# Kernel tuning notes

Measured on AMD Instinct MI355X. Metric: run time of the kernel, lower is better.

The kernel has to match this reference:

```python
import jax, jax.numpy as jnp
import numpy as np

EPS = 1e-5
GROUPS = 4


def gconv1x1(x, w, b, groups):
    # x: [B,C,H,W]; w: [Cout, Cin//groups]; grouped 1x1 conv
    B, C, H, W = x.shape
    Co = w.shape[0]
    xg = x.reshape(B, groups, C // groups, H, W)
    wg = w.reshape(groups, Co // groups, C // groups)
    y = jnp.einsum('bgchw,goc->bgohw', xg, wg).reshape(B, Co, H, W)
    if b is not None:
        y = y + b[None, :, None, None]
    return y


def setup_inputs() -> dict:
    key = jax.random.key(0)
    ks = jax.random.split(key, 9)
    B, C, H, W = 8, 64, 160, 160
    Cq = C // 8
    s = 0.1
    return {
        'x': jax.random.normal(ks[0], (B, C, H, W), jnp.float32),
        'wq': jax.random.normal(ks[1], (Cq, C // GROUPS), jnp.float32) * s,
        'bq': jax.random.normal(ks[2], (Cq,), jnp.float32) * s,
        'wk': jax.random.normal(ks[3], (Cq, C // GROUPS), jnp.float32) * s,
        'bk': jax.random.normal(ks[4], (Cq,), jnp.float32) * s,
        'wv': jax.random.normal(ks[5], (C, C // GROUPS), jnp.float32) * s,
        'bv': jax.random.normal(ks[6], (C,), jnp.float32) * s,
        'gamma': jax.random.normal(ks[7], (1,), jnp.float32) * s,
        'w1d': jax.random.normal(ks[8], (C, C // GROUPS), jnp.float32) * s,
        'bn_w': jnp.ones((C,), jnp.float32),
        'bn_b': jnp.zeros((C,), jnp.float32),
    }


def reference(x, wq, bq, wk, bk, wv, bv, gamma, w1d, bn_w, bn_b):
    B, C, H, W = x.shape
    q = gconv1x1(x, wq, bq, GROUPS)   # [B,Cq,H,W]
    k = gconv1x1(x, wk, bk, GROUPS)   # [B,Cq,H,W]
    v = gconv1x1(x, wv, bv, GROUPS)   # [B,C,H,W]

    # column (H) attention energies with -inf diagonal (self excluded on H path)
    energy_H = jnp.einsum('bchw,bcjw->bhwj', q, k)  # [B,H,W,H]
    diag = jnp.where(jnp.eye(H, dtype=bool), -jnp.inf, 0.0).astype(x.dtype)
    energy_H = energy_H + diag[:, None, :]
    # row (W) attention energies
    energy_W = jnp.einsum('bchw,bchj->bhwj', q, k)  # [B,H,W,W]

    att = jax.nn.softmax(jnp.concatenate([energy_H, energy_W], axis=3), axis=3)
    att_H = att[..., :H]           # [B,H,W,H]
    att_W = att[..., H:]           # [B,H,W,W]

    out_H = jnp.einsum('bcjw,bhwj->bchw', v, att_H)
    out_W = jnp.einsum('bchj,bhwj->bchw', v, att_W)
    out = gamma[0] * (out_H + out_W)               # [B,C,H,W]

    # kernel-size-1 grouped conv1d (dilation irrelevant for k=1), no bias
    L = H * W
    o = out.reshape(B, GROUPS, C // GROUPS, L)
    w1g = w1d.reshape(GROUPS, C // GROUPS, C // GROUPS)
    o = jnp.einsum('bgcl,goc->bgol', o, w1g).reshape(B, C, L)

    # BatchNorm1d (training mode: batch stats over (B, L), biased variance)
    mean = jnp.mean(o, axis=(0, 2), keepdims=True)
    var = jnp.mean((o - mean) ** 2, axis=(0, 2), keepdims=True)
    o = (o - mean) / jnp.sqrt(var + EPS) * bn_w[None, :, None] + bn_b[None, :, None]

    o = o.reshape(B, C, H, W)
    return jax.nn.relu(o + x)
```

## Files before the change

### kernel.cpp

```cpp
#include <hip/hip_runtime.h>
#include <math.h>

#define B_ 8
#define C_ 64
#define H_ 160
#define W_ 160
#define HW_ (H_*W_)

typedef _Float16 h2 __attribute__((ext_vector_type(2)));
typedef _Float16 h8 __attribute__((ext_vector_type(8)));
typedef float f4v __attribute__((ext_vector_type(4)));
union H8u { h8 v; h2 h[4]; };

__device__ inline float fdot2(h2 a, h2 b, float c) {
    return __builtin_amdgcn_fdot2(a, b, c, false);
}
__device__ inline float dot16(const float4* xr, const float* wr, float acc) {
    float4 a = xr[0], b = xr[1], c = xr[2], d = xr[3];
    acc += a.x*wr[0]  + a.y*wr[1]  + a.z*wr[2]  + a.w*wr[3];
    acc += b.x*wr[4]  + b.y*wr[5]  + b.z*wr[6]  + b.w*wr[7];
    acc += c.x*wr[8]  + c.y*wr[9]  + c.z*wr[10] + c.w*wr[11];
    acc += d.x*wr[12] + d.y*wr[13] + d.z*wr[14] + d.w*wr[15];
    return acc;
}

static constexpr size_t N_PIX  = (size_t)B_*H_*W_;
static constexpr size_t N_FULL = (size_t)B_*H_*W_*C_;
static constexpr size_t OFF_OUTH  = 0;
static constexpr size_t OFF_VROW  = N_FULL/2;
static constexpr size_t OFF_QROW  = OFF_VROW + N_FULL/2;
static constexpr size_t OFF_KROW  = OFF_QROW + N_PIX*4;
static constexpr size_t OFF_MH    = OFF_KROW + N_PIX*4;
static constexpr size_t OFF_SH    = OFF_MH + N_PIX;
static constexpr size_t OFF_BNSUM = OFF_SH + N_PIX;
static constexpr size_t OFF_BNSQ  = OFF_BNSUM + 64;
static constexpr size_t OFF_SCALE = OFF_BNSQ + 64;
static constexpr size_t OFF_SHIFT = OFF_SCALE + 64;

__global__ __launch_bounds__(256,4) void qkv_kernel(
    const float* __restrict__ x,
    const float* __restrict__ wq, const float* __restrict__ bq,
    const float* __restrict__ wk, const float* __restrict__ bk,
    const float* __restrict__ wv, const float* __restrict__ bv,
    _Float16* __restrict__ qrow, _Float16* __restrict__ krow,
    _Float16* __restrict__ vrow)
{
    __shared__ __align__(16) float xs[128][68];
    const int tid = threadIdx.x;
    const int w0 = blockIdx.x * 32;
    const int h0 = blockIdx.y * 4;
    const int b  = blockIdx.z;

    const float* xb = x + (size_t)b*C_*HW_;
    for (int i = tid; i < 2048; i += 256) {
        int c = i >> 5, hh = (i >> 3) & 3, w4 = i & 7;
        float4 v = *(const float4*)(xb + (size_t)c*HW_ + (size_t)(h0+hh)*W_ + w0 + w4*4);
        int pix = hh*32 + w4*4;
        xs[pix+0][c] = v.x; xs[pix+1][c] = v.y; xs[pix+2][c] = v.z; xs[pix+3][c] = v.w;
    }
    __syncthreads();

    float resv[32];
    {
        const int cp = tid & 31, pg = tid >> 5;
        const int c0 = 2*cp, g = c0 >> 4;
        float w0r[16], w1r[16];
        #pragma unroll
        for (int p = 0; p < 4; p++) {
            *(float4*)&w0r[4*p] = ((const float4*)(wv + c0*16))[p];
            *(float4*)&w1r[4*p] = ((const float4*)(wv + (c0+1)*16))[p];
        }
        const float b0 = bv[c0], b1 = bv[c0+1];
        #pragma unroll 4
        for (int i = 0; i < 16; i++) {
            int pix = pg*16 + i;
            const float4* xr = (const float4*)&xs[pix][g*16];
            resv[2*i]   = dot16(xr, w0r, b0);
            resv[2*i+1] = dot16(xr, w1r, b1);
        }
    }
    float resqk[8];
    {
        const int out = tid & 15, pg = tid >> 4;
        const int cq = out & 7, g = cq >> 1;
        const float* wp = ((out < 8) ? wq : wk) + cq*16;
        const float bb = (out < 8) ? bq[cq] : bk[cq];
        float wr[16];
        #pragma unroll
        for (int p = 0; p < 4; p++) *(float4*)&wr[4*p] = ((const float4*)wp)[p];
        #pragma unroll
        for (int i = 0; i < 8; i++) {
            int pix = pg*8 + i;
            resqk[i] = dot16((const float4*)&xs[pix][g*16], wr, bb);
        }
    }
    __syncthreads();

    unsigned* vs32 = (unsigned*)&xs[0][0];
    unsigned* qk32 = vs32 + 4096;
    {
        const int cp = tid & 31, pg = tid >> 5;
        #pragma unroll
        for (int i = 0; i < 16; i++) {
            int pix = pg*16 + i;
            h2 p; p.x = (_Float16)resv[2*i]; p.y = (_Float16)resv[2*i+1];
            vs32[pix*32 + cp] = *(unsigned*)&p;
        }
    }
    {
        const int out = tid & 15, pg = tid >> 4;
        _Float16* qks = (_Float16*)qk32;
        #pragma unroll
        for (int i = 0; i < 8; i++) qks[(pg*8+i)*16 + out] = (_Float16)resqk[i];
    }
    __syncthreads();

    unsigned* vrow32 = (unsigned*)vrow;
    for (int i = tid; i < 4096; i += 256) {
        int pix = i >> 5, cp = i & 31;
        size_t bp = ((size_t)b*H_ + h0 + (pix>>5))*W_ + w0 + (pix & 31);
        vrow32[bp*32 + cp] = vs32[i];
    }
    unsigned* qrow32 = (unsigned*)qrow;
    unsigned* krow32 = (unsigned*)krow;
    for (int i = tid; i < 1024; i += 256) {
        int pix = i >> 3, part = i & 7;
        size_t bp = ((size_t)b*H_ + h0 + (pix>>5))*W_ + w0 + (pix & 31);
        unsigned val = qk32[pix*8 + part];
        if (part < 4) qrow32[bp*4 + part]     = val;
        else          krow32[bp*4 + part - 4] = val;
    }
}

__global__ __launch_bounds__(256,4) void passA_kernel(
    const _Float16* __restrict__ qrow, const _Float16* __restrict__ krow,
    const _Float16* __restrict__ vrow,
    _Float16* __restrict__ outH, float* __restrict__ mH, float* __restrict__ sH)
{
    __shared__ __align__(16) h2 v2[64][84];
    __shared__ __align__(16) _Float16 q2h[160][8];
    __shared__ __align__(16) _Float16 k2h[160][8];
    __shared__ __align__(16) h2 Pt[32][84];

    const int tid = threadIdx.x;
    const int b = blockIdx.x / W_;
    const int w = blockIdx.x % W_;

    if (tid < 160) {
        size_t bp = ((size_t)b*H_ + tid)*W_ + w;
        *(int4*)&q2h[tid][0] = *(const int4*)(qrow + bp*8);
        *(int4*)&k2h[tid][0] = *(const int4*)(krow + bp*8);
    }
    {
        const unsigned* vr32 = (const unsigned*)vrow;
        const int cp = tid & 31, hp0 = tid >> 5;
        #pragma unroll 2
        for (int it = 0; it < 10; it++) {
            int hp = hp0 + 8*it;
            size_t bp0 = (size_t)b*HW_ + (size_t)(2*hp)*W_ + w;
            unsigned u0 = vr32[bp0*32 + cp];
            unsigned u1 = vr32[(bp0 + W_)*32 + cp];
            unsigned e  = __builtin_amdgcn_perm(u1, u0, 0x05040100);
            unsigned o  = __builtin_amdgcn_perm(u1, u0, 0x07060302);
            *(unsigned*)&v2[2*cp][hp]   = e;
            *(unsigned*)&v2[2*cp+1][hp] = o;
        }
    }
    __syncthreads();

    const int u    = tid & 7;
    const int wl   = tid >> 3;
    const int lane = tid & 63;
    const int wid  = tid >> 6;
    const int cM   = wid*16 + (lane & 15);
    const int m_   = lane & 15;
    const int dq   = lane >> 4;

    for (int t = 0; t < 5; t++) {
        const int qh = t*32 + wl;
        H8u qr; qr.v = *(const h8*)&q2h[qh][0];
        float ev[20];
        float mloc = -1e30f;
        #pragma unroll 2
        for (int p = 0; p < 10; p++) {
            int j0 = 2*(u + 8*p);
            H8u ka; ka.v = *(const h8*)&k2h[j0][0];
            H8u kb; kb.v = *(const h8*)&k2h[j0+1][0];
            float e0 = 0.f, e1 = 0.f;
            #pragma unroll
            for (int i = 0; i < 4; i++) {
                e0 = fdot2(qr.h[i], ka.h[i], e0);
                e1 = fdot2(qr.h[i], kb.h[i], e1);
            }
            ev[2*p] = e0; ev[2*p+1] = e1;
            if (j0   != qh) mloc = fmaxf(mloc, e0);
            if (j0+1 != qh) mloc = fmaxf(mloc, e1);
        }
        mloc = fmaxf(mloc, __shfl_xor(mloc, 1));
        mloc = fmaxf(mloc, __shfl_xor(mloc, 2));
        mloc = fmaxf(mloc, __shfl_xor(mloc, 4));
        float sloc = 0.f;
        #pragma unroll
        for (int p = 0; p < 10; p++) {
            int j0 = 2*(u + 8*p);
            float p0 = (j0   == qh) ? 0.f : __expf(ev[2*p]   - mloc);
            float p1 = (j0+1 == qh) ? 0.f : __expf(ev[2*p+1] - mloc);
            sloc += p0 + p1;
            h2 pp; pp.x = (_Float16)p0; pp.y = (_Float16)p1;
            Pt[wl][u + 8*p] = pp;
        }
        sloc += __shfl_xor(sloc, 1);
        sloc += __shfl_xor(sloc, 2);
        sloc += __shfl_xor(sloc, 4);
        if (u == 0) {
            mH[((size_t)b*W_ + w)*H_ + qh] = mloc;
            sH[((size_t)b*W_ + w)*H_ + qh] = sloc;
        }
        __syncthreads();

        f4v acc0 = {0.f,0.f,0.f,0.f}, acc1 = {0.f,0.f,0.f,0.f};
        #pragma unroll
        for (int kt = 0; kt < 5; kt++) {
            const int off = 64*kt + 16*dq;
            h8 bfr = *(const h8*)((const char*)&v2[cM][0] + off);
            h8 a0  = *(const h8*)((const char*)&Pt[m_][0] + off);
            h8 a1  = *(const h8*)((const char*)&Pt[16 + m_][0] + off);
            acc0 = __builtin_amdgcn_mfma_f32_16x16x32_f16(a0, bfr, acc0, 0, 0, 0);
            acc1 = __builtin_amdgcn_mfma_f32_16x16x32_f16(a1, bfr, acc1, 0, 0, 0);
        }
        #pragma unroll
        for (int r = 0; r < 4; r++) {
            int r0 = t*32 + dq*4 + r;
            outH[(((size_t)b*H_ + r0     )*W_ + w)*64 + cM] = (_Float16)acc0[r];
            outH[(((size_t)b*H_ + r0 + 16)*W_ + w)*64 + cM] = (_Float16)acc1[r];
        }
        __syncthreads();
    }
}

__global__ __launch_bounds__(256,4) void passB_kernel(
    const _Float16* __restrict__ qrow, const _Float16* __restrict__ krow,
    const _Float16* vrow,
    const float* __restrict__ gamma, const float* __restrict__ w1d,
    const _Float16* __restrict__ outH, const float* __restrict__ mH, const float* __restrict__ sH,
    _Float16* o16, float* __restrict__ bnsum, float* __restrict__ bnsq)
{
    __shared__ __align__(16) h2 v2[64][84];
    __shared__ __align__(16) _Float16 q2h[160][8];
    __shared__ __align__(16) _Float16 k2h[160][8];
    __shared__ __align__(16) h2 Pt[32][84];
    __shared__ float fHs[32], fWs[32];

    const int tid = threadIdx.x;
    const int b = blockIdx.x / H_;
    const int h = blockIdx.x % H_;
    const float gam = gamma[0];

    const int lane = tid & 63;
    const int wid  = tid >> 6;
    const int cM   = wid*16 + (lane & 15);
    const int m_   = lane & 15;
    const int dq   = lane >> 4;

    float w1dr[16];
    #pragma unroll
    for (int p = 0; p < 4; p++) *(float4*)&w1dr[4*p] = ((const float4*)(w1d + cM*16))[p];

    const size_t rowbase = ((size_t)b*H_ + h)*W_;
    if (tid < 160) {
        size_t bp = rowbase + tid;
        *(int4*)&q2h[tid][0] = *(const int4*)(qrow + bp*8);
        *(int4*)&k2h[tid][0] = *(const int4*)(krow + bp*8);
    }
    {
        const unsigned* vr32 = (const unsigned*)vrow;
        const int cp = tid & 31, wp0 = tid >> 5;
        #pragma unroll 2
        for (int it = 0; it < 10; it++) {
            int wp = wp0 + 8*it;
            size_t bp0 = rowbase + 2*wp;
            unsigned u0 = vr32[bp0*32 + cp];
            unsigned u1 = vr32[(bp0 + 1)*32 + cp];
            unsigned e  = __builtin_amdgcn_perm(u1, u0, 0x05040100);
            unsigned o  = __builtin_amdgcn_perm(u1, u0, 0x07060302);
            *(unsigned*)&v2[2*cp][wp]   = e;
            *(unsigned*)&v2[2*cp+1][wp] = o;
        }
    }
    __syncthreads();

    const int u  = tid & 7;
    const int wl = tid >> 3;
    float bnS = 0.f, bnS2 = 0.f;

    for (int t = 0; t < 5; t++) {
        float oh0[4], oh1[4];
        #pragma unroll
        for (int r = 0; r < 4; r++) {
            int rw0 = t*32 + dq*4 + r;
            oh0[r] = (float)outH[(rowbase + rw0     )*64 + cM];
            oh1[r] = (float)outH[(rowbase + rw0 + 16)*64 + cM];
        }

        const int qw = t*32 + wl;
        H8u qr; qr.v = *(const h8*)&q2h[qw][0];
        float ev[20];
        float mloc = -1e30f;
        #pragma unroll 2
        for (int p = 0; p < 10; p++) {
            int j0 = 2*(u + 8*p);
            H8u ka; ka.v = *(const h8*)&k2h[j0][0];
            H8u kb; kb.v = *(const h8*)&k2h[j0+1][0];
            float e0 = 0.f, e1 = 0.f;
            #pragma unroll
            for (int i = 0; i < 4; i++) {
                e0 = fdot2(qr.h[i], ka.h[i], e0);
                e1 = fdot2(qr.h[i], kb.h[i], e1);
            }
            ev[2*p] = e0; ev[2*p+1] = e1;
            mloc = fmaxf(mloc, e0);
            mloc = fmaxf(mloc, e1);
        }
        mloc = fmaxf(mloc, __shfl_xor(mloc, 1));
        mloc = fmaxf(mloc, __shfl_xor(mloc, 2));
        mloc = fmaxf(mloc, __shfl_xor(mloc, 4));
        float sloc = 0.f;
        #pragma unroll
        for (int p = 0; p < 10; p++) {
            float p0 = __expf(ev[2*p]   - mloc);
            float p1 = __expf(ev[2*p+1] - mloc);
            sloc += p0 + p1;
            h2 pp; pp.x = (_Float16)p0; pp.y = (_Float16)p1;
            Pt[wl][u + 8*p] = pp;
        }
        sloc += __shfl_xor(sloc, 1);
        sloc += __shfl_xor(sloc, 2);
        sloc += __shfl_xor(sloc, 4);
        if (u == 0) {
            float mHv = mH[((size_t)b*W_ + qw)*H_ + h];
            float sHv = sH[((size_t)b*W_ + qw)*H_ + h];
            float M   = fmaxf(mHv, mloc);
            float eH  = __expf(mHv - M), eW = __expf(mloc - M);
            float inv = gam / (sHv*eH + sloc*eW);
            fHs[wl] = eH * inv;
            fWs[wl] = eW * inv;
        }
        __syncthreads();

        f4v acc0 = {0.f,0.f,0.f,0.f}, acc1 = {0.f,0.f,0.f,0.f};
        #pragma unroll
        for (int kt = 0; kt < 5; kt++) {
            const int off = 64*kt + 16*dq;
            h8 bfr = *(const h8*)((const char*)&v2[cM][0] + off);
            h8 a0  = *(const h8*)((const char*)&Pt[m_][0] + off);
            h8 a1  = *(const h8*)((const char*)&Pt[16 + m_][0] + off);
            acc0 = __builtin_amdgcn_mfma_f32_16x16x32_f16(a0, bfr, acc0, 0, 0, 0);
            acc1 = __builtin_amdgcn_mfma_f32_16x16x32_f16(a1, bfr, acc1, 0, 0, 0);
        }
        __syncthreads();

        float* stage = (float*)&Pt[0][0];
        #pragma unroll
        for (int r = 0; r < 4; r++) {
            int rl0 = dq*4 + r, rl1 = rl0 + 16;
            stage[rl0*68 + cM] = oh0[r]*fHs[rl0] + acc0[r]*fWs[rl0];
            stage[rl1*68 + cM] = oh1[r]*fHs[rl1] + acc1[r]*fWs[rl1];
        }
        #pragma unroll
        for (int r = 0; r < 4; r++) {
            #pragma unroll
            for (int mt = 0; mt < 2; mt++) {
                int rl = dq*4 + r + 16*mt;
                int rw = t*32 + rl;
                const float4* sp = (const float4*)&stage[rl*68 + 16*wid];
                float o = 0.f;
                #pragma unroll
                for (int p = 0; p < 4; p++) {
                    float4 sv = sp[p];
                    o += sv.x*w1dr[4*p] + sv.y*w1dr[4*p+1] + sv.z*w1dr[4*p+2] + sv.w*w1dr[4*p+3];
                }
                o16[(rowbase + rw)*64 + cM] = (_Float16)o;
                bnS  += o;
                bnS2 += o*o;
            }
        }
        __syncthreads();
    }
    bnS  += __shfl_xor(bnS, 16);  bnS  += __shfl_xor(bnS, 32);
    bnS2 += __shfl_xor(bnS2, 16); bnS2 += __shfl_xor(bnS2, 32);
    if (dq == 0) {
        atomicAdd(&bnsum[cM], bnS);
        atomicAdd(&bnsq[cM],  bnS2);
    }
}

__global__ void bnfin_kernel(const float* __restrict__ sum, const float* __restrict__ sq,
                             const float* __restrict__ bn_w, const float* __restrict__ bn_b,
                             float* __restrict__ scale, float* __restrict__ shift)
{
    int c = threadIdx.x;
    if (c < C_) {
        const float cnt = (float)(B_*H_*W_);
        float mean = sum[c] / cnt;
        float var  = sq[c] / cnt - mean*mean;
        float istd = rsqrtf(var + 1e-5f);
        float scl  = bn_w[c] * istd;
        scale[c] = scl;
        shift[c] = bn_b[c] - mean*scl;
    }
}

__global__ __launch_bounds__(256) void final_kernel(
    const float* __restrict__ x, const _Float16* __restrict__ o16,
    const float* __restrict__ scale, const float* __restrict__ shift,
    float* __restrict__ out)
{
    __shared__ _Float16 olds[160*66];
    __shared__ float sc[64], sh[64];
    const int tid = threadIdx.x;
    const int b = blockIdx.x / H_, h = blockIdx.x % H_;
    if (tid < 64) { sc[tid] = scale[tid]; sh[tid] = shift[tid]; }
    const unsigned* op = (const unsigned*)(o16 + ((size_t)b*H_ + h)*W_*64);
    unsigned* ol32 = (unsigned*)olds;
    for (int i = tid; i < 5120; i += 256) {
        int w = i >> 5, c2 = i & 31;
        ol32[w*33 + c2] = op[i];
    }
    __syncthreads();
    const float* xr = x   + (size_t)b*C_*HW_ + (size_t)h*W_;
    float*       ob = out + (size_t)b*C_*HW_ + (size_t)h*W_;
    for (int i = tid; i < 64*160; i += 256) {
        int c = i / 160, w = i - c*160;
        float v = (float)olds[w*66 + c] * sc[c] + sh[c] + xr[(size_t)c*HW_ + w];
        ob[(size_t)c*HW_ + w] = fmaxf(v, 0.f);
    }
}

extern "C" void kernel_launch(void* const* d_in, const int* in_sizes, int n_in,
                              void* d_out, int out_size, void* d_ws, size_t ws_size,
                              hipStream_t stream)
{
    (void)in_sizes; (void)n_in; (void)out_size; (void)ws_size;
    const float* x     = (const float*)d_in[0];
    const float* wq    = (const float*)d_in[1];
    const float* bq    = (const float*)d_in[2];
    const float* wk    = (const float*)d_in[3];
    const float* bk    = (const float*)d_in[4];
    const float* wv    = (const float*)d_in[5];
    const float* bv    = (const float*)d_in[6];
    const float* gamma = (const float*)d_in[7];
    const float* w1d   = (const float*)d_in[8];
    const float* bn_w  = (const float*)d_in[9];
    const float* bn_b  = (const float*)d_in[10];

    float* ws = (float*)d_ws;
    _Float16* outH16 = (_Float16*)(ws + OFF_OUTH);
    _Float16* vrow   = (_Float16*)(ws + OFF_VROW);
    _Float16* qrow   = (_Float16*)(ws + OFF_QROW);
    _Float16* krow   = (_Float16*)(ws + OFF_KROW);
    float* mH    = ws + OFF_MH;
    float* sH    = ws + OFF_SH;
    float* bnsum = ws + OFF_BNSUM;
    float* bnsq  = ws + OFF_BNSQ;
    float* scale = ws + OFF_SCALE;
    float* shift = ws + OFF_SHIFT;
    _Float16* o16 = vrow;

    hipMemsetAsync(bnsum, 0, 128*sizeof(float), stream);

    dim3 qgrid(W_/32, H_/4, B_);
    qkv_kernel<<<qgrid, 256, 0, stream>>>(x, wq, bq, wk, bk, wv, bv, qrow, krow, vrow);
    passA_kernel<<<B_*W_, 256, 0, stream>>>(qrow, krow, vrow, outH16, mH, sH);
    passB_kernel<<<B_*H_, 256, 0, stream>>>(qrow, krow, vrow, gamma, w1d,
                                            outH16, mH, sH, o16, bnsum, bnsq);
    bnfin_kernel<<<1, 64, 0, stream>>>(bnsum, bnsq, bn_w, bn_b, scale, shift);
    final_kernel<<<B_*H_, 256, 0, stream>>>(x, o16, scale, shift, (float*)d_out);
}
```

Baseline: 252.5 us.

## Retile LDS fragments for MFMA, stage conv in fp16 per wave, fold BN finalize

After: 244.0 us. 3.4% less time.

```diff
diff --git a/kernel.cpp b/kernel.cpp
--- a/kernel.cpp
+++ b/kernel.cpp
@@ -34,8 +34,6 @@
 static constexpr size_t OFF_SH    = OFF_MH + N_PIX;
 static constexpr size_t OFF_BNSUM = OFF_SH + N_PIX;
 static constexpr size_t OFF_BNSQ  = OFF_BNSUM + 64;
-static constexpr size_t OFF_SCALE = OFF_BNSQ + 64;
-static constexpr size_t OFF_SHIFT = OFF_SCALE + 64;
 
 __global__ __launch_bounds__(256,4) void qkv_kernel(
     const float* __restrict__ x,
@@ -53,7 +51,9 @@
 
     const float* xb = x + (size_t)b*C_*HW_;
     for (int i = tid; i < 2048; i += 256) {
-        int c = i >> 5, hh = (i >> 3) & 3, w4 = i & 7;
+        int w4 = i & 7;
+        int c  = ((i >> 3) & 7) | (((i >> 6) & 7) << 3);
+        int hh = i >> 9;
         float4 v = *(const float4*)(xb + (size_t)c*HW_ + (size_t)(h0+hh)*W_ + w0 + w4*4);
         int pix = hh*32 + w4*4;
         xs[pix+0][c] = v.x; xs[pix+1][c] = v.y; xs[pix+2][c] = v.z; xs[pix+3][c] = v.w;
@@ -137,10 +137,10 @@
     const _Float16* __restrict__ vrow,
     _Float16* __restrict__ outH, float* __restrict__ mH, float* __restrict__ sH)
 {
-    __shared__ __align__(16) h2 v2[64][84];
+    __shared__ __align__(16) _Float16 v2s[5*4*64*8];
+    __shared__ __align__(16) _Float16 Pts[5*4*32*8];
     __shared__ __align__(16) _Float16 q2h[160][8];
     __shared__ __align__(16) _Float16 k2h[160][8];
-    __shared__ __align__(16) h2 Pt[32][84];
 
     const int tid = threadIdx.x;
     const int b = blockIdx.x / W_;
@@ -157,13 +157,15 @@
         #pragma unroll 2
         for (int it = 0; it < 10; it++) {
             int hp = hp0 + 8*it;
-            size_t bp0 = (size_t)b*HW_ + (size_t)(2*hp)*W_ + w;
+            int kt = hp >> 4, dqv = (hp >> 2) & 3, jj = 2*(hp & 3);
+            size_t bp0 = ((size_t)b*H_ + 2*hp)*W_ + w;
             unsigned u0 = vr32[bp0*32 + cp];
             unsigned u1 = vr32[(bp0 + W_)*32 + cp];
             unsigned e  = __builtin_amdgcn_perm(u1, u0, 0x05040100);
             unsigned o  = __builtin_amdgcn_perm(u1, u0, 0x07060302);
-            *(unsigned*)&v2[2*cp][hp]   = e;
-            *(unsigned*)&v2[2*cp+1][hp] = o;
+            int base = ((kt*4 + dqv)*64 + 2*cp)*8 + jj;
+            *(unsigned*)&v2s[base]     = e;
+            *(unsigned*)&v2s[base + 8] = o;
         }
     }
     __syncthreads();
@@ -183,7 +185,7 @@
         float mloc = -1e30f;
         #pragma unroll 2
         for (int p = 0; p < 10; p++) {
-            int j0 = 2*(u + 8*p);
+            int j0 = 2*u + 16*p;
             H8u ka; ka.v = *(const h8*)&k2h[j0][0];
             H8u kb; kb.v = *(const h8*)&k2h[j0+1][0];
             float e0 = 0.f, e1 = 0.f;
@@ -202,12 +204,13 @@
         float sloc = 0.f;
         #pragma unroll
         for (int p = 0; p < 10; p++) {
-            int j0 = 2*(u + 8*p);
+            int j0 = 2*u + 16*p;
             float p0 = (j0   == qh) ? 0.f : __expf(ev[2*p]   - mloc);
             float p1 = (j0+1 == qh) ? 0.f : __expf(ev[2*p+1] - mloc);
             sloc += p0 + p1;
             h2 pp; pp.x = (_Float16)p0; pp.y = (_Float16)p1;
-            Pt[wl][u + 8*p] = pp;
+            int idx = (((p>>1)*4 + (u>>2) + 2*(p&1))*32 + wl)*8 + 2*(u&3);
+            *(unsigned*)&Pts[idx] = *(unsigned*)&pp;
         }
         sloc += __shfl_xor(sloc, 1);
         sloc += __shfl_xor(sloc, 2);
@@ -221,10 +224,9 @@
         f4v acc0 = {0.f,0.f,0.f,0.f}, acc1 = {0.f,0.f,0.f,0.f};
         #pragma unroll
         for (int kt = 0; kt < 5; kt++) {
-            const int off = 64*kt + 16*dq;
-            h8 bfr = *(const h8*)((const char*)&v2[cM][0] + off);
-            h8 a0  = *(const h8*)((const char*)&Pt[m_][0] + off);
-            h8 a1  = *(const h8*)((const char*)&Pt[16 + m_][0] + off);
+            h8 bfr = *(const h8*)&v2s[((kt*4 + dq)*64 + cM)*8];
+            h8 a0  = *(const h8*)&Pts[((kt*4 + dq)*32 + m_)*8];
+            h8 a1  = *(const h8*)&Pts[((kt*4 + dq)*32 + 16 + m_)*8];
             acc0 = __builtin_amdgcn_mfma_f32_16x16x32_f16(a0, bfr, acc0, 0, 0, 0);
             acc1 = __builtin_amdgcn_mfma_f32_16x16x32_f16(a1, bfr, acc1, 0, 0, 0);
         }
@@ -245,10 +247,11 @@
     const _Float16* __restrict__ outH, const float* __restrict__ mH, const float* __restrict__ sH,
     _Float16* o16, float* __restrict__ bnsum, float* __restrict__ bnsq)
 {
-    __shared__ __align__(16) h2 v2[64][84];
+    __shared__ __align__(16) _Float16 v2s[5*4*64*8];
+    __shared__ __align__(16) _Float16 Pts[5*4*32*8];
     __shared__ __align__(16) _Float16 q2h[160][8];
     __shared__ __align__(16) _Float16 k2h[160][8];
-    __shared__ __align__(16) h2 Pt[32][84];
+    __shared__ __align__(16) _Float16 stageh[4*32*18];
     __shared__ float fHs[32], fWs[32];
 
     const int tid = threadIdx.x;
@@ -262,9 +265,13 @@
     const int m_   = lane & 15;
     const int dq   = lane >> 4;
 
-    float w1dr[16];
+    h2 w1h[8];
     #pragma unroll
-    for (int p = 0; p < 4; p++) *(float4*)&w1dr[4*p] = ((const float4*)(w1d + cM*16))[p];
+    for (int p = 0; p < 8; p++) {
+        float2 wpair = ((const float2*)(w1d + cM*16))[p];
+        h2 wp; wp.x = (_Float16)wpair.x; wp.y = (_Float16)wpair.y;
+        w1h[p] = wp;
+    }
 
     const size_t rowbase = ((size_t)b*H_ + h)*W_;
     if (tid < 160) {
@@ -278,13 +285,15 @@
         #pragma unroll 2
         for (int it = 0; it < 10; it++) {
             int wp = wp0 + 8*it;
+            int kt = wp >> 4, dqv = (wp >> 2) & 3, jj = 2*(wp & 3);
             size_t bp0 = rowbase + 2*wp;
             unsigned u0 = vr32[bp0*32 + cp];
             unsigned u1 = vr32[(bp0 + 1)*32 + cp];
             unsigned e  = __builtin_amdgcn_perm(u1, u0, 0x05040100);
             unsigned o  = __builtin_amdgcn_perm(u1, u0, 0x07060302);
-            *(unsigned*)&v2[2*cp][wp]   = e;
-            *(unsigned*)&v2[2*cp+1][wp] = o;
+            int base = ((kt*4 + dqv)*64 + 2*cp)*8 + jj;
+            *(unsigned*)&v2s[base]     = e;
+            *(unsigned*)&v2s[base + 8] = o;
         }
     }
     __syncthreads();
@@ -308,7 +317,7 @@
         float mloc = -1e30f;
         #pragma unroll 2
         for (int p = 0; p < 10; p++) {
-            int j0 = 2*(u + 8*p);
+            int j0 = 2*u + 16*p;
             H8u ka; ka.v = *(const h8*)&k2h[j0][0];
             H8u kb; kb.v = *(const h8*)&k2h[j0+1][0];
             float e0 = 0.f, e1 = 0.f;
@@ -331,7 +340,8 @@
             float p1 = __expf(ev[2*p+1] - mloc);
             sloc += p0 + p1;
             h2 pp; pp.x = (_Float16)p0; pp.y = (_Float16)p1;
-            Pt[wl][u + 8*p] = pp;
+            int idx = (((p>>1)*4 + (u>>2) + 2*(p&1))*32 + wl)*8 + 2*(u&3);
+            *(unsigned*)&Pts[idx] = *(unsigned*)&pp;
         }
         sloc += __shfl_xor(sloc, 1);
         sloc += __shfl_xor(sloc, 2);
@@ -350,21 +360,18 @@
         f4v acc0 = {0.f,0.f,0.f,0.f}, acc1 = {0.f,0.f,0.f,0.f};
         #pragma unroll
         for (int kt = 0; kt < 5; kt++) {
-            const int off = 64*kt + 16*dq;
-            h8 bfr = *(const h8*)((const char*)&v2[cM][0] + off);
-            h8 a0  = *(const h8*)((const char*)&Pt[m_][0] + off);
-            h8 a1  = *(const h8*)((const char*)&Pt[16 + m_][0] + off);
+            h8 bfr = *(const h8*)&v2s[((kt*4 + dq)*64 + cM)*8];
+            h8 a0  = *(const h8*)&Pts[((kt*4 + dq)*32 + m_)*8];
+            h8 a1  = *(const h8*)&Pts[((kt*4 + dq)*32 + 16 + m_)*8];
             acc0 = __builtin_amdgcn_mfma_f32_16x16x32_f16(a0, bfr, acc0, 0, 0, 0);
             acc1 = __builtin_amdgcn_mfma_f32_16x16x32_f16(a1, bfr, acc1, 0, 0, 0);
         }
-        __syncthreads();
-
-        float* stage = (float*)&Pt[0][0];
+        _Float16* st = &stageh[wid*576];
         #pragma unroll
         for (int r = 0; r < 4; r++) {
             int rl0 = dq*4 + r, rl1 = rl0 + 16;
-            stage[rl0*68 + cM] = oh0[r]*fHs[rl0] + acc0[r]*fWs[rl0];
-            stage[rl1*68 + cM] = oh1[r]*fHs[rl1] + acc1[r]*fWs[rl1];
+            st[rl0*18 + m_] = (_Float16)(oh0[r]*fHs[rl0] + acc0[r]*fWs[rl0]);
+            st[rl1*18 + m_] = (_Float16)(oh1[r]*fHs[rl1] + acc1[r]*fWs[rl1]);
         }
         #pragma unroll
         for (int r = 0; r < 4; r++) {
@@ -372,13 +379,10 @@
             for (int mt = 0; mt < 2; mt++) {
                 int rl = dq*4 + r + 16*mt;
                 int rw = t*32 + rl;
-                const float4* sp = (const float4*)&stage[rl*68 + 16*wid];
+                const h2* sp = (const h2*)&st[rl*18];
                 float o = 0.f;
                 #pragma unroll
-                for (int p = 0; p < 4; p++) {
-                    float4 sv = sp[p];
-                    o += sv.x*w1dr[4*p] + sv.y*w1dr[4*p+1] + sv.z*w1dr[4*p+2] + sv.w*w1dr[4*p+3];
-                }
+                for (int p = 0; p < 8; p++) o = fdot2(sp[p], w1h[p], o);
                 o16[(rowbase + rw)*64 + cM] = (_Float16)o;
                 bnS  += o;
                 bnS2 += o*o;
@@ -394,32 +398,25 @@
     }
 }
 
-__global__ void bnfin_kernel(const float* __restrict__ sum, const float* __restrict__ sq,
-                             const float* __restrict__ bn_w, const float* __restrict__ bn_b,
-                             float* __restrict__ scale, float* __restrict__ shift)
-{
-    int c = threadIdx.x;
-    if (c < C_) {
-        const float cnt = (float)(B_*H_*W_);
-        float mean = sum[c] / cnt;
-        float var  = sq[c] / cnt - mean*mean;
-        float istd = rsqrtf(var + 1e-5f);
-        float scl  = bn_w[c] * istd;
-        scale[c] = scl;
-        shift[c] = bn_b[c] - mean*scl;
-    }
-}
-
 __global__ __launch_bounds__(256) void final_kernel(
     const float* __restrict__ x, const _Float16* __restrict__ o16,
-    const float* __restrict__ scale, const float* __restrict__ shift,
+    const float* __restrict__ bnsum, const float* __restrict__ bnsq,
+    const float* __restrict__ bn_w, const float* __restrict__ bn_b,
     float* __restrict__ out)
 {
     __shared__ _Float16 olds[160*66];
     __shared__ float sc[64], sh[64];
     const int tid = threadIdx.x;
     const int b = blockIdx.x / H_, h = blockIdx.x % H_;
-    if (tid < 64) { sc[tid] = scale[tid]; sh[tid] = shift[tid]; }
+    if (tid < 64) {
+        const float cnt = (float)(B_*H_*W_);
+        float mean = bnsum[tid] / cnt;
+        float var  = bnsq[tid] / cnt - mean*mean;
+        float istd = rsqrtf(var + 1e-5f);
+        float scl  = bn_w[tid] * istd;
+        sc[tid] = scl;
+        sh[tid] = bn_b[tid] - mean*scl;
+    }
     const unsigned* op = (const unsigned*)(o16 + ((size_t)b*H_ + h)*W_*64);
     unsigned* ol32 = (unsigned*)olds;
     for (int i = tid; i < 5120; i += 256) {
@@ -462,8 +459,6 @@
     float* sH    = ws + OFF_SH;
     float* bnsum = ws + OFF_BNSUM;
     float* bnsq  = ws + OFF_BNSQ;
-    float* scale = ws + OFF_SCALE;
-    float* shift = ws + OFF_SHIFT;
     _Float16* o16 = vrow;
 
     hipMemsetAsync(bnsum, 0, 128*sizeof(float), stream);
@@ -473,6 +468,5 @@
     passA_kernel<<<B_*W_, 256, 0, stream>>>(qrow, krow, vrow, outH16, mH, sH);
     passB_kernel<<<B_*H_, 256, 0, stream>>>(qrow, krow, vrow, gamma, w1d,
                                             outH16, mH, sH, o16, bnsum, bnsq);
-    bnfin_kernel<<<1, 64, 0, stream>>>(bnsum, bnsq, bn_w, bn_b, scale, shift);
-    final_kernel<<<B_*H_, 256, 0, stream>>>(x, o16, scale, shift, (float*)d_out);
-}
+    final_kernel<<<B_*H_, 256, 0, stream>>>(x, o16, bnsum, bnsq, bn_w, bn_b, (float*)d_out);
+}
```
